# Kernel optimization log

Hardware: AMD Instinct MI355X
Metric: run time of the kernel (lower is better)

The kernel has to match this reference:

```python
import jax, jax.numpy as jnp
import numpy as np

VTH = 1.0      # v_threshold
TAU = 2.0      # spikingjelly LIFNode default tau
ALPHA = 2.0    # ATan surrogate alpha
EPS = 1e-5     # BatchNorm eps
N_HEADS = 8
TOPK = 4       # routed regions per query region
REGION = 64    # tokens per region (4096 tokens -> 64 regions)


@jax.custom_vjp
def spike_fn(v):
    return (v >= VTH).astype(v.dtype)

def _spike_fwd(v):
    return (v >= VTH).astype(v.dtype), v

def _spike_bwd(v, g):
    sg = (ALPHA / 2.0) / (1.0 + (jnp.pi / 2.0 * ALPHA * (v - VTH)) ** 2)
    return (g * sg,)

spike_fn.defvjp(_spike_fwd, _spike_bwd)


def lif(x):
    # x: [T, B, L, D]; LIF with decay_input=True, hard reset to 0, detach_reset
    def step(v, xt):
        v = v + (xt - v) / TAU
        s = spike_fn(v)
        v = v * (1.0 - jax.lax.stop_gradient(s))
        return v, s
    _, s = jax.lax.scan(step, jnp.zeros_like(x[0]), x)
    return s


def batchnorm(x, gamma, beta):
    # torch BN1d over [T*B, D, L] in training mode == per-channel stats over (T,B,L)
    mean = x.mean(axis=(0, 1, 2))
    var = jnp.mean((x - mean) ** 2, axis=(0, 1, 2))
    return (x - mean) * jax.lax.rsqrt(var + EPS) * gamma + beta


def bilevel_attn(x, qkv_w, qkv_b, proj_w, proj_b):
    # x: [TB, L, D]
    TB, L, D = x.shape
    nreg = L // REGION
    hd = D // N_HEADS
    qkv = x @ qkv_w.T + qkv_b
    q, k, v = jnp.split(qkv, 3, axis=-1)
    qr = q.reshape(TB, nreg, REGION, D)
    kr = k.reshape(TB, nreg, REGION, D)
    vr = v.reshape(TB, nreg, REGION, D)
    # coarse region-level routing via mean-pooled q/k affinity
    aff = jnp.einsum('bnd,bmd->bnm', qr.mean(2), kr.mean(2))  # [TB, nreg, nreg]
    _, idx = jax.lax.top_k(aff, TOPK)                         # [TB, nreg, TOPK]
    gather = jax.vmap(lambda t, ix: t[ix])                    # per-sample region gather
    kg = gather(kr, idx).reshape(TB, nreg, TOPK * REGION, N_HEADS, hd)
    vg = gather(vr, idx).reshape(TB, nreg, TOPK * REGION, N_HEADS, hd)
    qh = qr.reshape(TB, nreg, REGION, N_HEADS, hd)
    logits = jnp.einsum('bnqhd,bnkhd->bnhqk', qh, kg) * (hd ** -0.5)
    p = jax.nn.softmax(logits, axis=-1)
    o = jnp.einsum('bnhqk,bnkhd->bnqhd', p, vg).reshape(TB, L, D)
    return o @ proj_w.T + proj_b


def setup_inputs() -> dict:
    key = jax.random.key(0)
    ks = jax.random.split(key, 8)
    T, B, Lt, L, D = 4, 2, 4, 1024, 256
    Ltot = Lt * L
    s = 0.02
    return {
        'x': jax.random.normal(ks[0], (T, B, Ltot, D), jnp.float32),
        'bn1_g': jnp.ones((D,), jnp.float32),
        'bn1_b': jnp.zeros((D,), jnp.float32),
        'bn2_g': jnp.ones((D,), jnp.float32),
        'bn2_b': jnp.zeros((D,), jnp.float32),
        'qkv_w': jax.random.normal(ks[1], (3 * D, D), jnp.float32) * s,
        'qkv_b': jnp.zeros((3 * D,), jnp.float32),
        'proj_w': jax.random.normal(ks[2], (D, D), jnp.float32) * s,
        'proj_b': jnp.zeros((D,), jnp.float32),
        'ffn_w1': jax.random.normal(ks[3], (4 * D, D), jnp.float32) * s,
        'ffn_b1': jnp.zeros((4 * D,), jnp.float32),
        'ffn_w2': jax.random.normal(ks[4], (D, 4 * D), jnp.float32) * s,
        'ffn_b2': jnp.zeros((D,), jnp.float32),
        'scale': jnp.ones((1,), jnp.float32) * 0.5,
        'Lt': Lt, 'b': B, 'L': L, 'dim': D,
    }


def reference(x, bn1_g, bn1_b, bn2_g, bn2_b, qkv_w, qkv_b, proj_w, proj_b,
              ffn_w1, ffn_b1, ffn_w2, ffn_b2, scale, Lt, b, L, dim):
    T = x.shape[0]
    Ltot = Lt * L
    # attention branch
    identity = x
    s1 = lif(batchnorm(x, bn1_g, bn1_b))
    a = bilevel_attn(s1.reshape(T * b, Ltot, dim), qkv_w, qkv_b, proj_w, proj_b)
    x = identity + a.reshape(T, b, Ltot, dim) * scale
    # ffn branch
    s2 = lif(batchnorm(x, bn2_g, bn2_b))
    h = jax.nn.gelu(s2 @ ffn_w1.T + ffn_b1, approximate=False) @ ffn_w2.T + ffn_b2
    return x + h * scale
```

## Files before the change

### kernel.cpp

```cpp
#include <hip/hip_runtime.h>
#include <hip/hip_bf16.h>
#include <math.h>

typedef __attribute__((ext_vector_type(8))) short short8;
typedef __attribute__((ext_vector_type(4))) float f32x4;

#define DIM 256
#define NROWS 32768
#define PERT 2097152
#define SAMP_TOK 4096

__device__ __forceinline__ float b2f(__hip_bfloat16 h){ return __bfloat162float(h); }
__device__ __forceinline__ __hip_bfloat16 f2b(float f){ return __float2bfloat16(f); }
__device__ __forceinline__ unsigned short f2bu(float f){
  __hip_bfloat16 h = __float2bfloat16(f);
  unsigned short u; __builtin_memcpy(&u, &h, 2); return u;
}

#define GLD_LDS16(gp, lp) __builtin_amdgcn_global_load_lds( \
    (const __attribute__((address_space(1))) unsigned int*)(gp), \
    (__attribute__((address_space(3))) unsigned int*)(lp), 16, 0, 0)

__device__ __forceinline__ float gelu_fast(float v){
  float z  = v * 0.70710678118654752f;
  float az = fabsf(z);
  float t  = __builtin_amdgcn_rcpf(fmaf(0.3275911f, az, 1.0f));
  float p  = fmaf(fmaf(fmaf(fmaf(1.061405429f, t, -1.453152027f), t,
                            1.421413741f), t, -0.284496736f), t, 0.254829592f);
  p *= t;
  float e  = __expf(-z * z);
  float y  = fmaf(-p, e, 1.0f);
  return fmaf(0.5f * fabsf(v), y, 0.5f * v);
}

__global__ void f2ball_k(const float* __restrict__ w_qkv, const float* __restrict__ w_proj,
                         const float* __restrict__ w_f1, const float* __restrict__ w_f2,
                         __hip_bfloat16* __restrict__ o_qkv, __hip_bfloat16* __restrict__ o_proj,
                         __hip_bfloat16* __restrict__ o_f1, __hip_bfloat16* __restrict__ o_f2){
  int i = blockIdx.x * 256 + threadIdx.x;
  if (i < 196608)          o_qkv[i]           = f2b(w_qkv[i]);
  else if (i < 262144)     o_proj[i - 196608] = f2b(w_proj[i - 196608]);
  else if (i < 524288)     o_f1[i - 262144]   = f2b(w_f1[i - 262144]);
  else                     o_f2[i - 524288]   = f2b(w_f2[i - 524288]);
}

__global__ void bn_stats_k(const float* __restrict__ x, float* __restrict__ sum, float* __restrict__ sumsq){
  int c = threadIdx.x;
  size_t base = (size_t)blockIdx.x * 64 * DIM + c;
  float s = 0.f, s2 = 0.f;
  for (int i = 0; i < 64; ++i){
    float v = x[base + (size_t)i * DIM];
    s += v; s2 += v * v;
  }
  atomicAdd(&sum[c], s);
  atomicAdd(&sumsq[c], s2);
}

__global__ void bn_fin_k(const float* __restrict__ sum, const float* __restrict__ sumsq,
                         const float* __restrict__ g, const float* __restrict__ b,
                         float* __restrict__ a_out, float* __restrict__ b_out){
  int c = threadIdx.x;
  float mean = sum[c] * (1.f/32768.f);
  float var  = sumsq[c] * (1.f/32768.f) - mean*mean;
  float a = g[c] / sqrtf(var + 1e-5f);
  a_out[c] = a;
  b_out[c] = b[c] - mean * a;
}

__global__ void lif_k(const float* __restrict__ x, const float* __restrict__ av,
                      const float* __restrict__ bv, __hip_bfloat16* __restrict__ s){
  int e = blockIdx.x * blockDim.x + threadIdx.x;
  if (e >= PERT) return;
  int c = e & (DIM - 1);
  float a = av[c], b = bv[c];
  float v = 0.f;
  #pragma unroll
  for (int t = 0; t < 4; ++t){
    float xn = x[(size_t)t * PERT + e] * a + b;
    v += (xn - v) * 0.5f;
    float sp = (v >= 1.0f) ? 1.0f : 0.0f;
    s[(size_t)t * PERT + e] = f2b(sp);
    v = (v >= 1.0f) ? 0.f : v;
  }
}

__global__ void region_sum_k(const __hip_bfloat16* __restrict__ s, float* __restrict__ sm){
  int r = blockIdx.x, c = threadIdx.x;
  float acc = 0.f;
  size_t base = (size_t)r * 64 * DIM + c;
  for (int i = 0; i < 64; ++i) acc += b2f(s[base + (size_t)i * DIM]);
  sm[(size_t)r * DIM + c] = acc * 0.015625f;
}

__global__ void rgemm_k(const float* __restrict__ smr, const float* __restrict__ w,
                        const float* __restrict__ bias, float* __restrict__ qkm){
  __shared__ float arow[256];
  int r = blockIdx.x, t = threadIdx.x;
  arow[t] = smr[(size_t)r * 256 + t];
  __syncthreads();
  for (int j = t; j < 512; j += 256){
    const float* wr = w + (size_t)j * 256;
    float acc = 0.f;
    for (int k = 0; k < 256; ++k) acc += arow[k] * wr[k];
    qkm[(size_t)r * 512 + j] = acc + bias[j];
  }
}

template<int EPI>
__global__ __launch_bounds__(256) void gemm_bt(
    const __hip_bfloat16* __restrict__ A, const __hip_bfloat16* __restrict__ W,
    const float* __restrict__ bias, void* __restrict__ outp,
    const void* __restrict__ extra, const float* __restrict__ scaleptr,
    int K, int N)
{
  __shared__ __align__(16) short As0[128 * 32];
  __shared__ __align__(16) short Ws0[128 * 32];
  __shared__ __align__(16) short As1[128 * 32];
  __shared__ __align__(16) short Ws1[128 * 32];
  int tid = threadIdx.x;
  int bm = blockIdx.x, bn = blockIdx.y;
  int lane = tid & 63;
  int l16 = lane & 15, quad = lane >> 4;
  int wv = tid >> 6;
  int wm = (wv >> 1) << 6, wn = (wv & 1) << 6;

  const int srow = tid >> 2;
  const int sq   = (tid & 3) ^ ((srow >> 1) & 3);
  const __hip_bfloat16* Ag = A + (size_t)(bm * 128 + srow) * K + (sq << 3);
  const __hip_bfloat16* Wg = W + (size_t)(bn * 128 + srow) * K + (sq << 3);
  const size_t rstep = (size_t)64 * K;

  int roA[4], roW[4];
  #pragma unroll
  for (int i = 0; i < 4; ++i){
    int Ra = wm + i * 16 + l16;
    roA[i] = Ra * 32 + ((quad ^ ((Ra >> 1) & 3)) << 3);
    int Rw = wn + i * 16 + l16;
    roW[i] = Rw * 32 + ((quad ^ ((Rw >> 1) & 3)) << 3);
  }

  f32x4 zero = {0.f, 0.f, 0.f, 0.f};
  f32x4 acc[4][4];
  #pragma unroll
  for (int i = 0; i < 4; ++i)
    #pragma unroll
    for (int j = 0; j < 4; ++j) acc[i][j] = zero;

  auto stage = [&](short* Ad, short* Wd, int k0){
    GLD_LDS16(Ag + k0,         Ad + tid * 8);
    GLD_LDS16(Ag + rstep + k0, Ad + tid * 8 + 2048);
    GLD_LDS16(Wg + k0,         Wd + tid * 8);
    GLD_LDS16(Wg + rstep + k0, Wd + tid * 8 + 2048);
  };
  auto compute = [&](const short* Asb, const short* Wsb){
    short8 af[4];
    #pragma unroll
    for (int mi = 0; mi < 4; ++mi)
      af[mi] = *reinterpret_cast<const short8*>(Asb + roA[mi]);
    #pragma unroll
    for (int ni = 0; ni < 4; ++ni){
      short8 wf = *reinterpret_cast<const short8*>(Wsb + roW[ni]);
      #pragma unroll
      for (int mi = 0; mi < 4; ++mi)
        acc[mi][ni] = __builtin_amdgcn_mfma_f32_16x16x32_bf16(wf, af[mi], acc[mi][ni], 0, 0, 0);
    }
  };

  stage(As0, Ws0, 0);
  __syncthreads();
  for (int k0 = 0; k0 < K; k0 += 64){
    if (k0 + 32 < K) stage(As1, Ws1, k0 + 32);
    compute(As0, Ws0);
    __syncthreads();
    if (k0 + 64 < K) stage(As0, Ws0, k0 + 64);
    if (k0 + 32 < K) compute(As1, Ws1);
    __syncthreads();
  }

  if (EPI == 0 || EPI == 2){
    short* Cw = (wv == 0) ? As0 : (wv == 1) ? Ws0 : (wv == 2) ? As1 : Ws1;
    #pragma unroll
    for (int ni = 0; ni < 4; ++ni){
      int col0 = (bn << 7) + wn + ni * 16 + (quad << 2);
      float4 bv = *reinterpret_cast<const float4*>(bias + col0);
      #pragma unroll
      for (int mi = 0; mi < 4; ++mi){
        float v0 = acc[mi][ni][0] + bv.x;
        float v1 = acc[mi][ni][1] + bv.y;
        float v2 = acc[mi][ni][2] + bv.z;
        float v3 = acc[mi][ni][3] + bv.w;
        if (EPI == 2){
          v0 = gelu_fast(v0); v1 = gelu_fast(v1);
          v2 = gelu_fast(v2); v3 = gelu_fast(v3);
        }
        unsigned lo = (unsigned)f2bu(v0) | ((unsigned)f2bu(v1) << 16);
        unsigned hi = (unsigned)f2bu(v2) | ((unsigned)f2bu(v3) << 16);
        int row = mi * 16 + l16;
        int cb  = (ni * 32 + (quad << 3)) ^ ((row & 7) << 4);
        *reinterpret_cast<uint2*>(reinterpret_cast<char*>(Cw) + row * 128 + cb) =
            make_uint2(lo, hi);
      }
    }
    asm volatile("s_waitcnt lgkmcnt(0)" ::: "memory");
    #pragma unroll
    for (int p = 0; p < 8; ++p){
      int row = p * 8 + (lane >> 3);
      int cb  = ((lane & 7) << 4) ^ ((row & 7) << 4);
      uint4 val = *reinterpret_cast<const uint4*>(
          reinterpret_cast<const char*>(Cw) + row * 128 + cb);
      int rowg = (bm << 7) + wm + row;
      int colg = (bn << 7) + wn + ((lane & 7) << 3);
      *reinterpret_cast<uint4*>((__hip_bfloat16*)outp + (size_t)rowg * N + colg) = val;
    }
  } else {
    float sc = scaleptr[0];
    #pragma unroll
    for (int ni = 0; ni < 4; ++ni){
      int col0 = (bn << 7) + wn + ni * 16 + (quad << 2);
      float4 bv = *reinterpret_cast<const float4*>(bias + col0);
      #pragma unroll
      for (int mi = 0; mi < 4; ++mi){
        int rowg = (bm << 7) + wm + mi * 16 + l16;
        size_t off = (size_t)rowg * N + col0;
        float v0 = acc[mi][ni][0] + bv.x;
        float v1 = acc[mi][ni][1] + bv.y;
        float v2 = acc[mi][ni][2] + bv.z;
        float v3 = acc[mi][ni][3] + bv.w;
        float4 xr = *reinterpret_cast<const float4*>((const float*)extra + off);
        float4 ov;
        ov.x = xr.x + v0 * sc; ov.y = xr.y + v1 * sc;
        ov.z = xr.z + v2 * sc; ov.w = xr.w + v3 * sc;
        *reinterpret_cast<float4*>((float*)outp + off) = ov;
      }
    }
  }
}

__global__ void topk_k(const float* __restrict__ qkm, int* __restrict__ idx){
  __shared__ float aff[64];
  int r = blockIdx.x;
  int m = threadIdx.x;
  int b = r >> 6;
  const float4* qrow = reinterpret_cast<const float4*>(qkm + (size_t)r * 512);
  const float4* krow = reinterpret_cast<const float4*>(qkm + (size_t)(b * 64 + m) * 512 + 256);
  float dot = 0.f;
  for (int d = 0; d < 64; ++d){
    float4 qv = qrow[d], kv = krow[d];
    dot += qv.x * kv.x + qv.y * kv.y + qv.z * kv.z + qv.w * kv.w;
  }
  aff[m] = dot;
  __syncthreads();
  if (m == 0){
    #pragma unroll
    for (int t = 0; t < 4; ++t){
      float best = -INFINITY; int bi = 0;
      for (int i = 0; i < 64; ++i){
        if (aff[i] > best){ best = aff[i]; bi = i; }
      }
      aff[bi] = -INFINITY;
      idx[r * 4 + t] = bi;
    }
  }
}

__global__ __launch_bounds__(256) void attn_mfma_k(
    const __hip_bfloat16* __restrict__ qkv, const int* __restrict__ idx,
    __hip_bfloat16* __restrict__ o_out, int rbase)
{
  __shared__ __align__(16) short lds[27136];
  const int rl = blockIdx.x;
  const int h  = blockIdx.y;
  const int rg = rbase + rl;
  const int bl = rl >> 6;
  const int tid = threadIdx.x;
  const int w = tid >> 6, lane = tid & 63;
  const int l16 = lane & 15, quad = lane >> 4;
  short* Pw = lds + 10240 + w * 4224;

  const int reg = idx[rg * 4 + (tid >> 6)] & 63;
  const size_t srow = (size_t)bl * SAMP_TOK + (size_t)reg * 64 + (tid & 63);
  const __hip_bfloat16* kvsrc = qkv + srow * 768 + 256 + (size_t)h * 32;

  const size_t qrow = (size_t)rl * 64 + w * 16 + l16;
  short8 qf = *reinterpret_cast<const short8*>(qkv + qrow * 768 + (size_t)h * 32 + quad * 8);

  uint4 vreg[4];
  #pragma unroll
  for (int c = 0; c < 4; ++c)
    vreg[c] = *reinterpret_cast<const uint4*>(kvsrc + 256 + c * 8);

  #pragma unroll
  for (int c = 0; c < 4; ++c)
    *reinterpret_cast<uint4*>(&lds[tid * 40 + c * 8]) =
      *reinterpret_cast<const uint4*>(kvsrc + c * 8);
  __syncthreads();

  f32x4 s[16];
  #pragma unroll
  for (int nt = 0; nt < 16; ++nt){
    short8 kf = *reinterpret_cast<const short8*>(&lds[(nt * 16 + l16) * 40 + quad * 8]);
    f32x4 z = {0.f, 0.f, 0.f, 0.f};
    s[nt] = __builtin_amdgcn_mfma_f32_16x16x32_bf16(kf, qf, z, 0, 0, 0);
  }
  __syncthreads();

  #pragma unroll
  for (int c = 0; c < 4; ++c){
    short8 vv = *reinterpret_cast<short8*>(&vreg[c]);
    #pragma unroll
    for (int e = 0; e < 8; ++e)
      lds[(c * 8 + e) * 264 + tid] = vv[e];
  }

  float mx = -1e30f;
  #pragma unroll
  for (int nt = 0; nt < 16; ++nt)
    #pragma unroll
    for (int r = 0; r < 4; ++r) mx = fmaxf(mx, s[nt][r]);
  mx = fmaxf(mx, __shfl_xor(mx, 16));
  mx = fmaxf(mx, __shfl_xor(mx, 32));
  float den = 0.f;
  #pragma unroll
  for (int nt = 0; nt < 16; ++nt)
    #pragma unroll
    for (int r = 0; r < 4; ++r){
      float e = __expf((s[nt][r] - mx) * 0.17677669529663687f);
      s[nt][r] = e; den += e;
    }
  den += __shfl_xor(den, 16);
  den += __shfl_xor(den, 32);

  #pragma unroll
  for (int nt = 0; nt < 16; ++nt){
    unsigned lo = (unsigned)f2bu(s[nt][0]) | ((unsigned)f2bu(s[nt][1]) << 16);
    unsigned hi = (unsigned)f2bu(s[nt][2]) | ((unsigned)f2bu(s[nt][3]) << 16);
    *reinterpret_cast<uint2*>(&Pw[l16 * 264 + nt * 16 + quad * 4]) = make_uint2(lo, hi);
  }
  __syncthreads();

  f32x4 o0 = {0.f, 0.f, 0.f, 0.f}, o1 = o0;
  #pragma unroll
  for (int kk = 0; kk < 8; ++kk){
    short8 pb = *reinterpret_cast<const short8*>(&Pw[l16 * 264 + kk * 32 + quad * 8]);
    short8 a0 = *reinterpret_cast<const short8*>(&lds[l16 * 264 + kk * 32 + quad * 8]);
    short8 a1 = *reinterpret_cast<const short8*>(&lds[(16 + l16) * 264 + kk * 32 + quad * 8]);
    o0 = __builtin_amdgcn_mfma_f32_16x16x32_bf16(a0, pb, o0, 0, 0, 0);
    o1 = __builtin_amdgcn_mfma_f32_16x16x32_bf16(a1, pb, o1, 0, 0, 0);
  }
  float inv = 1.f / den;
  size_t obase = ((size_t)rl * 64 + w * 16 + l16) * 256 + (size_t)h * 32;
  unsigned pk0 = (unsigned)f2bu(o0[0] * inv) | ((unsigned)f2bu(o0[1] * inv) << 16);
  unsigned pk1 = (unsigned)f2bu(o0[2] * inv) | ((unsigned)f2bu(o0[3] * inv) << 16);
  unsigned pk2 = (unsigned)f2bu(o1[0] * inv) | ((unsigned)f2bu(o1[1] * inv) << 16);
  unsigned pk3 = (unsigned)f2bu(o1[2] * inv) | ((unsigned)f2bu(o1[3] * inv) << 16);
  *reinterpret_cast<uint2*>(o_out + obase + quad * 4)      = make_uint2(pk0, pk1);
  *reinterpret_cast<uint2*>(o_out + obase + 16 + quad * 4) = make_uint2(pk2, pk3);
}

extern "C" void kernel_launch(void* const* d_in, const int* in_sizes, int n_in,
                              void* d_out, int out_size, void* d_ws, size_t ws_size,
                              hipStream_t stream)
{
  const float* x      = (const float*)d_in[0];
  const float* bn1_g  = (const float*)d_in[1];
  const float* bn1_b  = (const float*)d_in[2];
  const float* bn2_g  = (const float*)d_in[3];
  const float* bn2_b  = (const float*)d_in[4];
  const float* qkv_w  = (const float*)d_in[5];
  const float* qkv_b  = (const float*)d_in[6];
  const float* proj_w = (const float*)d_in[7];
  const float* proj_b = (const float*)d_in[8];
  const float* ffn_w1 = (const float*)d_in[9];
  const float* ffn_b1 = (const float*)d_in[10];
  const float* ffn_w2 = (const float*)d_in[11];
  const float* ffn_b2 = (const float*)d_in[12];
  const float* scale  = (const float*)d_in[13];
  float* x2 = (float*)d_out;

  char* ws = (char*)d_ws;
  const size_t MB = 1024 * 1024;
  float* sum1 = (float*)(ws + 0);
  float* sq1  = (float*)(ws + 1024);
  float* sum2 = (float*)(ws + 2048);
  float* sq2  = (float*)(ws + 3072);
  float* a1   = (float*)(ws + 4096);
  float* b1   = (float*)(ws + 5120);
  float* a2   = (float*)(ws + 6144);
  float* b2   = (float*)(ws + 7168);
  int*   idxb = (int*)(ws + 8192);
  float* smr  = (float*)(ws + 16384);
  float* qkm  = (float*)(ws + 540672);
  __hip_bfloat16* qkv_wb  = (__hip_bfloat16*)(ws + 1589248);
  __hip_bfloat16* proj_wb = (__hip_bfloat16*)(ws + 1982464);
  __hip_bfloat16* ffn_w1b = (__hip_bfloat16*)(ws + 2113536);
  __hip_bfloat16* ffn_w2b = (__hip_bfloat16*)(ws + 2637824);
  __hip_bfloat16* s1 = (__hip_bfloat16*)(ws + 4 * MB);
  __hip_bfloat16* s2 = s1;
  char* chunkbuf = ws + 20 * MB;

  size_t avail = (ws_size > 20 * MB) ? (ws_size - 20 * MB) : (8 * MB);
  int nc = (avail >= 64 * MB) ? 8 : (avail >= 32 * MB) ? 4 : (avail >= 16 * MB) ? 2 : 1;
  int crows = 32768;
  while ((size_t)crows * 2048 > avail && crows > 2048) crows >>= 1;

  __hip_bfloat16* qkvc = (__hip_bfloat16*)chunkbuf;
  __hip_bfloat16* oc   = (__hip_bfloat16*)(chunkbuf + (size_t)nc * 6 * MB);
  __hip_bfloat16* h1   = (__hip_bfloat16*)chunkbuf;

  hipMemsetAsync(d_ws, 0, 4096, stream);

  f2ball_k<<<3072, 256, 0, stream>>>(qkv_w, proj_w, ffn_w1, ffn_w2,
                                     qkv_wb, proj_wb, ffn_w1b, ffn_w2b);

  bn_stats_k<<<512, 256, 0, stream>>>(x, sum1, sq1);
  bn_fin_k<<<1, 256, 0, stream>>>(sum1, sq1, bn1_g, bn1_b, a1, b1);
  lif_k<<<PERT / 256, 256, 0, stream>>>(x, a1, b1, s1);
  region_sum_k<<<512, 256, 0, stream>>>(s1, smr);
  rgemm_k<<<512, 256, 0, stream>>>(smr, qkv_w, qkv_b, qkm);
  topk_k<<<512, 64, 0, stream>>>(qkm, idxb);

  const int nchunkA = 8 / nc;
  for (int c = 0; c < nchunkA; ++c){
    const size_t ro = (size_t)c * nc * SAMP_TOK;
    gemm_bt<0><<<dim3(nc * SAMP_TOK / 128, 6), 256, 0, stream>>>(
        s1 + ro * 256, qkv_wb, qkv_b, qkvc, nullptr, nullptr, 256, 768);
    attn_mfma_k<<<dim3(nc * 64, 8), 256, 0, stream>>>(qkvc, idxb, oc, c * nc * 64);
    gemm_bt<1><<<dim3(nc * SAMP_TOK / 128, 2), 256, 0, stream>>>(
        oc, proj_wb, proj_b, x2 + ro * 256, x + ro * 256, scale, 256, 256);
  }

  bn_stats_k<<<512, 256, 0, stream>>>(x2, sum2, sq2);
  bn_fin_k<<<1, 256, 0, stream>>>(sum2, sq2, bn2_g, bn2_b, a2, b2);
  lif_k<<<PERT / 256, 256, 0, stream>>>(x2, a2, b2, s2);
  const int nchunkF = 32768 / crows;
  for (int c = 0; c < nchunkF; ++c){
    const size_t ro = (size_t)c * crows;
    gemm_bt<2><<<dim3(crows / 128, 8), 256, 0, stream>>>(
        s2 + ro * 256, ffn_w1b, ffn_b1, h1, nullptr, nullptr, 256, 1024);
    gemm_bt<3><<<dim3(crows / 128, 2), 256, 0, stream>>>(
        h1, ffn_w2b, ffn_b2, x2 + ro * 256, x2 + ro * 256, scale, 1024, 256);
  }
}
```

Baseline: 371.8 us.

## Fuse second BN statistics into proj GEMM epilogue and vectorize LIF/stat kernels

The second batch-norm statistics pass is folded into the projection GEMM epilogue: each output tile reduces its sums and squared sums with wave shuffles and atomically adds per-column partials, so the separate re-read of x2 is gone. The bn_stats, lif and region_sum kernels are rewritten to use float4/ushort4 vector loads, with shared-memory reductions in bn_stats and region_sum. The trade-off is more atomics and registers in the GEMM epilogue, plus a one-pass E[x^2]-mean^2 variance accumulated in a different order.

```diff
diff --git a/kernel.cpp b/kernel.cpp
--- a/kernel.cpp
+++ b/kernel.cpp
@@ -45,15 +45,23 @@
 }
 
 __global__ void bn_stats_k(const float* __restrict__ x, float* __restrict__ sum, float* __restrict__ sumsq){
-  int c = threadIdx.x;
-  size_t base = (size_t)blockIdx.x * 64 * DIM + c;
-  float s = 0.f, s2 = 0.f;
-  for (int i = 0; i < 64; ++i){
-    float v = x[base + (size_t)i * DIM];
-    s += v; s2 += v * v;
-  }
-  atomicAdd(&sum[c], s);
-  atomicAdd(&sumsq[c], s2);
+  __shared__ __align__(16) float rs[4][256];
+  __shared__ __align__(16) float rq[4][256];
+  int t = threadIdx.x;
+  int g = t & 63, r = t >> 6;
+  size_t base = ((size_t)blockIdx.x * 128 + r) * DIM + g * 4;
+  float4 s = {0.f,0.f,0.f,0.f}, q = {0.f,0.f,0.f,0.f};
+  for (int i = 0; i < 32; ++i){
+    float4 v = *reinterpret_cast<const float4*>(x + base + (size_t)i * 4 * DIM);
+    s.x += v.x; s.y += v.y; s.z += v.z; s.w += v.w;
+    q.x += v.x*v.x; q.y += v.y*v.y; q.z += v.z*v.z; q.w += v.w*v.w;
+  }
+  *reinterpret_cast<float4*>(&rs[r][g*4]) = s;
+  *reinterpret_cast<float4*>(&rq[r][g*4]) = q;
+  __syncthreads();
+  int c = t;
+  atomicAdd(&sum[c],   rs[0][c] + rs[1][c] + rs[2][c] + rs[3][c]);
+  atomicAdd(&sumsq[c], rq[0][c] + rq[1][c] + rq[2][c] + rq[3][c]);
 }
 
 __global__ void bn_fin_k(const float* __restrict__ sum, const float* __restrict__ sumsq,
@@ -69,27 +77,50 @@
 
 __global__ void lif_k(const float* __restrict__ x, const float* __restrict__ av,
                       const float* __restrict__ bv, __hip_bfloat16* __restrict__ s){
-  int e = blockIdx.x * blockDim.x + threadIdx.x;
-  if (e >= PERT) return;
-  int c = e & (DIM - 1);
-  float a = av[c], b = bv[c];
-  float v = 0.f;
+  int i = blockIdx.x * 256 + threadIdx.x;
+  int e4 = i * 4;
+  int c4 = e4 & (DIM - 1);
+  float4 a = *reinterpret_cast<const float4*>(av + c4);
+  float4 b = *reinterpret_cast<const float4*>(bv + c4);
+  float4 v = {0.f,0.f,0.f,0.f};
   #pragma unroll
   for (int t = 0; t < 4; ++t){
-    float xn = x[(size_t)t * PERT + e] * a + b;
-    v += (xn - v) * 0.5f;
-    float sp = (v >= 1.0f) ? 1.0f : 0.0f;
-    s[(size_t)t * PERT + e] = f2b(sp);
-    v = (v >= 1.0f) ? 0.f : v;
+    float4 xn = *reinterpret_cast<const float4*>(x + (size_t)t * PERT + e4);
+    xn.x = fmaf(xn.x, a.x, b.x); xn.y = fmaf(xn.y, a.y, b.y);
+    xn.z = fmaf(xn.z, a.z, b.z); xn.w = fmaf(xn.w, a.w, b.w);
+    v.x += (xn.x - v.x) * 0.5f; v.y += (xn.y - v.y) * 0.5f;
+    v.z += (xn.z - v.z) * 0.5f; v.w += (xn.w - v.w) * 0.5f;
+    ushort4 sp;
+    sp.x = (v.x >= 1.0f) ? 0x3F80 : 0;  v.x = (v.x >= 1.0f) ? 0.f : v.x;
+    sp.y = (v.y >= 1.0f) ? 0x3F80 : 0;  v.y = (v.y >= 1.0f) ? 0.f : v.y;
+    sp.z = (v.z >= 1.0f) ? 0x3F80 : 0;  v.z = (v.z >= 1.0f) ? 0.f : v.z;
+    sp.w = (v.w >= 1.0f) ? 0x3F80 : 0;  v.w = (v.w >= 1.0f) ? 0.f : v.w;
+    *reinterpret_cast<ushort4*>(reinterpret_cast<unsigned short*>(s) + (size_t)t * PERT + e4) = sp;
   }
 }
 
 __global__ void region_sum_k(const __hip_bfloat16* __restrict__ s, float* __restrict__ sm){
-  int r = blockIdx.x, c = threadIdx.x;
-  float acc = 0.f;
-  size_t base = (size_t)r * 64 * DIM + c;
-  for (int i = 0; i < 64; ++i) acc += b2f(s[base + (size_t)i * DIM]);
-  sm[(size_t)r * DIM + c] = acc * 0.015625f;
+  __shared__ __align__(16) float red[4][256];
+  int r = blockIdx.x, t = threadIdx.x;
+  int g = t & 63, sub = t >> 6;
+  const unsigned short* sp = reinterpret_cast<const unsigned short*>(s);
+  size_t base = ((size_t)r * 64 + sub * 16) * DIM + g * 4;
+  float4 acc = {0.f,0.f,0.f,0.f};
+  for (int i = 0; i < 16; ++i){
+    ushort4 u = *reinterpret_cast<const ushort4*>(sp + base + (size_t)i * DIM);
+    acc.x += (u.x != 0) ? 1.f : 0.f; acc.y += (u.y != 0) ? 1.f : 0.f;
+    acc.z += (u.z != 0) ? 1.f : 0.f; acc.w += (u.w != 0) ? 1.f : 0.f;
+  }
+  *reinterpret_cast<float4*>(&red[sub][g*4]) = acc;
+  __syncthreads();
+  if (sub == 0){
+    float4 o;
+    o.x = (red[0][g*4+0] + red[1][g*4+0] + red[2][g*4+0] + red[3][g*4+0]) * 0.015625f;
+    o.y = (red[0][g*4+1] + red[1][g*4+1] + red[2][g*4+1] + red[3][g*4+1]) * 0.015625f;
+    o.z = (red[0][g*4+2] + red[1][g*4+2] + red[2][g*4+2] + red[3][g*4+2]) * 0.015625f;
+    o.w = (red[0][g*4+3] + red[1][g*4+3] + red[2][g*4+3] + red[3][g*4+3]) * 0.015625f;
+    *reinterpret_cast<float4*>(sm + (size_t)r * DIM + g * 4) = o;
+  }
 }
 
 __global__ void rgemm_k(const float* __restrict__ smr, const float* __restrict__ w,
@@ -111,6 +142,7 @@
     const __hip_bfloat16* __restrict__ A, const __hip_bfloat16* __restrict__ W,
     const float* __restrict__ bias, void* __restrict__ outp,
     const void* __restrict__ extra, const float* __restrict__ scaleptr,
+    float* __restrict__ bsum, float* __restrict__ bsq,
     int K, int N)
 {
   __shared__ __align__(16) short As0[128 * 32];
@@ -214,6 +246,11 @@
     }
   } else {
     float sc = scaleptr[0];
+    float4 ts[4], tq[4];
+    if (EPI == 1){
+      #pragma unroll
+      for (int ni = 0; ni < 4; ++ni){ ts[ni] = {0.f,0.f,0.f,0.f}; tq[ni] = {0.f,0.f,0.f,0.f}; }
+    }
     #pragma unroll
     for (int ni = 0; ni < 4; ++ni){
       int col0 = (bn << 7) + wn + ni * 16 + (quad << 2);
@@ -231,6 +268,31 @@
         ov.x = xr.x + v0 * sc; ov.y = xr.y + v1 * sc;
         ov.z = xr.z + v2 * sc; ov.w = xr.w + v3 * sc;
         *reinterpret_cast<float4*>((float*)outp + off) = ov;
+        if (EPI == 1){
+          ts[ni].x += ov.x; ts[ni].y += ov.y; ts[ni].z += ov.z; ts[ni].w += ov.w;
+          tq[ni].x += ov.x*ov.x; tq[ni].y += ov.y*ov.y;
+          tq[ni].z += ov.z*ov.z; tq[ni].w += ov.w*ov.w;
+        }
+      }
+    }
+    if (EPI == 1){
+      #pragma unroll
+      for (int ni = 0; ni < 4; ++ni){
+        float4 S = ts[ni], Q = tq[ni];
+        #pragma unroll
+        for (int m = 1; m < 16; m <<= 1){
+          S.x += __shfl_xor(S.x, m); S.y += __shfl_xor(S.y, m);
+          S.z += __shfl_xor(S.z, m); S.w += __shfl_xor(S.w, m);
+          Q.x += __shfl_xor(Q.x, m); Q.y += __shfl_xor(Q.y, m);
+          Q.z += __shfl_xor(Q.z, m); Q.w += __shfl_xor(Q.w, m);
+        }
+        if (l16 == 0){
+          int col0 = (bn << 7) + wn + ni * 16 + (quad << 2);
+          atomicAdd(&bsum[col0+0], S.x); atomicAdd(&bsum[col0+1], S.y);
+          atomicAdd(&bsum[col0+2], S.z); atomicAdd(&bsum[col0+3], S.w);
+          atomicAdd(&bsq[col0+0], Q.x);  atomicAdd(&bsq[col0+1], Q.y);
+          atomicAdd(&bsq[col0+2], Q.z);  atomicAdd(&bsq[col0+3], Q.w);
+        }
       }
     }
   }
@@ -412,9 +474,9 @@
   f2ball_k<<<3072, 256, 0, stream>>>(qkv_w, proj_w, ffn_w1, ffn_w2,
                                      qkv_wb, proj_wb, ffn_w1b, ffn_w2b);
 
-  bn_stats_k<<<512, 256, 0, stream>>>(x, sum1, sq1);
+  bn_stats_k<<<256, 256, 0, stream>>>(x, sum1, sq1);
   bn_fin_k<<<1, 256, 0, stream>>>(sum1, sq1, bn1_g, bn1_b, a1, b1);
-  lif_k<<<PERT / 256, 256, 0, stream>>>(x, a1, b1, s1);
+  lif_k<<<PERT / 1024, 256, 0, stream>>>(x, a1, b1, s1);
   region_sum_k<<<512, 256, 0, stream>>>(s1, smr);
   rgemm_k<<<512, 256, 0, stream>>>(smr, qkv_w, qkv_b, qkm);
   topk_k<<<512, 64, 0, stream>>>(qkm, idxb);
@@ -423,21 +485,20 @@
   for (int c = 0; c < nchunkA; ++c){
     const size_t ro = (size_t)c * nc * SAMP_TOK;
     gemm_bt<0><<<dim3(nc * SAMP_TOK / 128, 6), 256, 0, stream>>>(
-        s1 + ro * 256, qkv_wb, qkv_b, qkvc, nullptr, nullptr, 256, 768);
+        s1 + ro * 256, qkv_wb, qkv_b, qkvc, nullptr, nullptr, nullptr, nullptr, 256, 768);
     attn_mfma_k<<<dim3(nc * 64, 8), 256, 0, stream>>>(qkvc, idxb, oc, c * nc * 64);
     gemm_bt<1><<<dim3(nc * SAMP_TOK / 128, 2), 256, 0, stream>>>(
-        oc, proj_wb, proj_b, x2 + ro * 256, x + ro * 256, scale, 256, 256);
-  }
-
-  bn_stats_k<<<512, 256, 0, stream>>>(x2, sum2, sq2);
+        oc, proj_wb, proj_b, x2 + ro * 256, x + ro * 256, scale, sum2, sq2, 256, 256);
+  }
+
   bn_fin_k<<<1, 256, 0, stream>>>(sum2, sq2, bn2_g, bn2_b, a2, b2);
-  lif_k<<<PERT / 256, 256, 0, stream>>>(x2, a2, b2, s2);
+  lif_k<<<PERT / 1024, 256, 0, stream>>>(x2, a2, b2, s2);
   const int nchunkF = 32768 / crows;
   for (int c = 0; c < nchunkF; ++c){
     const size_t ro = (size_t)c * crows;
     gemm_bt<2><<<dim3(crows / 128, 8), 256, 0, stream>>>(
-        s2 + ro * 256, ffn_w1b, ffn_b1, h1, nullptr, nullptr, 256, 1024);
+        s2 + ro * 256, ffn_w1b, ffn_b1, h1, nullptr, nullptr, nullptr, nullptr, 256, 1024);
     gemm_bt<3><<<dim3(crows / 128, 2), 256, 0, stream>>>(
-        h1, ffn_w2b, ffn_b2, x2 + ro * 256, x2 + ro * 256, scale, 1024, 256);
-  }
-}
+        h1, ffn_w2b, ffn_b2, x2 + ro * 256, x2 + ro * 256, scale, nullptr, nullptr, 1024, 256);
+  }
+}
```

After: 414.8 us. 1.12x slower.
